# Optimization experiments

Measured on AMD Instinct MI355X. Metric: run time of the kernel, lower is better.

The kernel has to match this reference:

```python
import jax, jax.numpy as jnp
import numpy as np

EMB = 256
HEADS = 8

def setup_inputs() -> dict:
    key = jax.random.key(0)
    ks = jax.random.split(key, 8)
    b, t, e, h = 8, 1024, EMB, HEADS
    x = jax.random.normal(ks[0], (b, t, e), dtype=jnp.float32)
    mask_idx = jax.random.randint(ks[1], (b, t, 1), 0, 2, dtype=jnp.int32)
    s = 1.0 / np.sqrt(e)
    Wq = jax.random.normal(ks[2], (e, e * h), dtype=jnp.float32) * s
    Wk = jax.random.normal(ks[3], (e, e * h), dtype=jnp.float32) * s
    Wv = jax.random.normal(ks[4], (e, e * h), dtype=jnp.float32) * s
    Wu = jax.random.normal(ks[5], (h * e, e), dtype=jnp.float32) * (1.0 / np.sqrt(h * e))
    bu = jnp.zeros((e,), dtype=jnp.float32)
    return {"x": x, "mask_idx": mask_idx, "Wq": Wq, "Wk": Wk, "Wv": Wv, "Wu": Wu, "bu": bu}

def reference(x, mask_idx, Wq, Wk, Wv, Wu, bu):
    b, t, e = x.shape
    h = HEADS
    # project and split heads: (b,t,h,e) -> (b,h,t,e)
    q = (x @ Wq).reshape(b, t, h, e).transpose(0, 2, 1, 3)
    k = (x @ Wk).reshape(b, t, h, e).transpose(0, 2, 1, 3)
    v = (x @ Wv).reshape(b, t, h, e).transpose(0, 2, 1, 3)
    scale = e ** 0.25
    q = q / scale
    k = k / scale
    dot = jnp.einsum('bhte,bhse->bhts', q, k)  # (b,h,t,t)
    m = mask_idx.astype(x.dtype)  # (b,t,1)
    mm = jnp.einsum('bti,bsi->bts', m, m)[:, None]  # (b,1,t,t), outer-product mask
    attn = jax.nn.softmax(dot * mm + (1.0 - mm) * (-1e30), axis=-1)
    out = jnp.einsum('bhts,bhse->bhte', attn, v)  # (b,h,t,e)
    out = out.transpose(0, 2, 1, 3).reshape(b, t, h * e)
    return out @ Wu + bu
```

## Files before the change

### kernel.cpp

```cpp
#include <hip/hip_runtime.h>

#define BB 8
#define TT 1024
#define EE 256
#define HH 8
#define BH 64
#define MM 8192
#define NQKV 2048

typedef __attribute__((ext_vector_type(8))) short bf16x8;
typedef __attribute__((ext_vector_type(4))) float f32x4;

__device__ __forceinline__ unsigned short f2bf(float f) {
  unsigned int u = __float_as_uint(f);
  u += 0x7fff + ((u >> 16) & 1);
  return (unsigned short)(u >> 16);
}

__global__ void k_convert_x(const float4* __restrict__ x, ushort4* __restrict__ xb, int n4) {
  int i = blockIdx.x * 256 + threadIdx.x;
  if (i < n4) {
    float4 f = x[i];
    ushort4 o;
    o.x = f2bf(f.x); o.y = f2bf(f.y); o.z = f2bf(f.z); o.w = f2bf(f.w);
    xb[i] = o;
  }
}

__global__ void k_transpose_w(const float* __restrict__ in, unsigned short* __restrict__ out,
                              int K, int N, float scale) {
  __shared__ float tile[32][33];
  int n0 = blockIdx.x * 32, k0 = blockIdx.y * 32;
  int tx = threadIdx.x & 31, ty = threadIdx.x >> 5;
#pragma unroll
  for (int p = 0; p < 4; p++) tile[ty + 8 * p][tx] = in[(size_t)(k0 + ty + 8 * p) * N + (n0 + tx)];
  __syncthreads();
#pragma unroll
  for (int p = 0; p < 4; p++)
    out[(size_t)(n0 + ty + 8 * p) * K + (k0 + tx)] = f2bf(scale * tile[tx][ty + 8 * p]);
}

__global__ __launch_bounds__(256) void k_gemm_qkv(
    const unsigned short* __restrict__ xb,
    const unsigned short* __restrict__ Wtq,
    const unsigned short* __restrict__ Wtk,
    const unsigned short* __restrict__ Wtv,
    unsigned short* __restrict__ qo,
    unsigned short* __restrict__ ko,
    unsigned short* __restrict__ vto) {
  __shared__ unsigned short sh[2 * 128 * 72];
  unsigned short* As = sh;
  unsigned short* Bs = sh + 128 * 72;
  const unsigned short* Bw = (blockIdx.z == 0) ? Wtq : (blockIdx.z == 1 ? Wtk : Wtv);
  int tid = threadIdx.x, lane = tid & 63, w = tid >> 6;
  int wr = w >> 1, wc = w & 1;
  int m0 = blockIdx.y * 128, n0 = blockIdx.x * 128;
  f32x4 acc[4][4] = {};
  for (int kt = 0; kt < 4; kt++) {
    __syncthreads();
    const unsigned short* ga = xb + (size_t)m0 * 256 + kt * 64;
    const unsigned short* gb = Bw + (size_t)n0 * 256 + kt * 64;
#pragma unroll
    for (int p = 0; p < 4; p++) {
      int c = p * 256 + tid, row = c >> 3, col = (c & 7) * 8;
      *(bf16x8*)&As[row * 72 + col] = *(const bf16x8*)&ga[(size_t)row * 256 + col];
      *(bf16x8*)&Bs[row * 72 + col] = *(const bf16x8*)&gb[(size_t)row * 256 + col];
    }
    __syncthreads();
#pragma unroll
    for (int kk = 0; kk < 2; kk++) {
      bf16x8 af[4], bfr[4];
#pragma unroll
      for (int mi = 0; mi < 4; mi++)
        af[mi] = *(bf16x8*)&As[(wr * 64 + mi * 16 + (lane & 15)) * 72 + kk * 32 + (lane >> 4) * 8];
#pragma unroll
      for (int ni = 0; ni < 4; ni++)
        bfr[ni] = *(bf16x8*)&Bs[(wc * 64 + ni * 16 + (lane & 15)) * 72 + kk * 32 + (lane >> 4) * 8];
#pragma unroll
      for (int mi = 0; mi < 4; mi++)
#pragma unroll
        for (int ni = 0; ni < 4; ni++)
          acc[mi][ni] = __builtin_amdgcn_mfma_f32_16x16x32_bf16(af[mi], bfr[ni], acc[mi][ni], 0, 0, 0);
    }
  }
  __syncthreads();
  unsigned short* ob = sh + w * (64 * 72);
  int gm0 = m0 + wr * 64, gn0 = n0 + wc * 64;
  int bb = gm0 >> 10, t0 = gm0 & 1023, hh = gn0 >> 8, d0 = gn0 & 255;
  if (blockIdx.z != 2) {
#pragma unroll
    for (int mi = 0; mi < 4; mi++)
#pragma unroll
      for (int ni = 0; ni < 4; ni++)
#pragma unroll
        for (int i = 0; i < 4; i++)
          ob[(mi * 16 + (lane >> 4) * 4 + i) * 72 + ni * 16 + (lane & 15)] = f2bf(acc[mi][ni][i]);
    unsigned short* outp = (blockIdx.z == 0) ? qo : ko;
    unsigned short* dst = outp + ((size_t)(bb * HH + hh) * TT + t0) * EE + d0;
#pragma unroll
    for (int p = 0; p < 8; p++) {
      int row = (lane >> 3) + 8 * p, col = (lane & 7) * 8;
      *(bf16x8*)&dst[(size_t)row * EE + col] = *(bf16x8*)&ob[row * 72 + col];
    }
  } else {
#pragma unroll
    for (int mi = 0; mi < 4; mi++)
#pragma unroll
      for (int ni = 0; ni < 4; ni++)
#pragma unroll
        for (int i = 0; i < 4; i++)
          ob[(ni * 16 + (lane & 15)) * 72 + mi * 16 + (lane >> 4) * 4 + i] = f2bf(acc[mi][ni][i]);
    unsigned short* dst = vto + ((size_t)(bb * HH + hh) * EE + d0) * TT + t0;
#pragma unroll
    for (int p = 0; p < 8; p++) {
      int row = (lane >> 3) + 8 * p, col = (lane & 7) * 8;
      *(bf16x8*)&dst[(size_t)row * TT + col] = *(bf16x8*)&ob[row * 72 + col];
    }
  }
}

__global__ __launch_bounds__(256, 2) void k_flash(
    const unsigned short* __restrict__ q,
    const unsigned short* __restrict__ k,
    const unsigned short* __restrict__ vt,
    const int* __restrict__ mask,
    unsigned short* __restrict__ ao) {
  __shared__ unsigned short Ks[64 * 264];
  __shared__ unsigned short Vs[256 * 72];
  __shared__ unsigned short Ps[4 * 16 * 72];
  int tid = threadIdx.x, lane = tid & 63, w = tid >> 6;
  int L = blockIdx.x;
  int wg = (L & 7) * 128 + (L >> 3);
  int qt = wg & 15, bh = wg >> 4;
  int b = bh >> 3, hh = bh & 7;
  const unsigned short* qbase = q + ((size_t)bh * TT + qt * 64) * EE;
  const unsigned short* kbase = k + (size_t)bh * TT * EE;
  const unsigned short* vbase = vt + (size_t)bh * EE * TT;

#pragma unroll
  for (int p = 0; p < 8; p++) {
    int c = p * 256 + tid, row = c >> 5, col = (c & 31) * 8;
    *(bf16x8*)&Ks[row * 264 + col] = *(const bf16x8*)&qbase[(size_t)row * EE + col];
  }
  __syncthreads();
  bf16x8 qr[8];
#pragma unroll
  for (int kk = 0; kk < 8; kk++)
    qr[kk] = *(bf16x8*)&Ks[(w * 16 + (lane & 15)) * 264 + kk * 32 + (lane >> 4) * 8];

  int mq[4];
#pragma unroll
  for (int i = 0; i < 4; i++)
    mq[i] = mask[b * TT + qt * 64 + w * 16 + (lane >> 4) * 4 + i];

  float mrow[4], lrow[4];
  f32x4 oacc[16] = {};
#pragma unroll
  for (int i = 0; i < 4; i++) { mrow[i] = -1e30f; lrow[i] = 0.0f; }

  for (int kt = 0; kt < 16; kt++) {
    __syncthreads();
#pragma unroll
    for (int p = 0; p < 8; p++) {
      int c = p * 256 + tid, row = c >> 5, col = (c & 31) * 8;
      *(bf16x8*)&Ks[row * 264 + col] = *(const bf16x8*)&kbase[((size_t)(kt * 64 + row)) * EE + col];
    }
#pragma unroll
    for (int p = 0; p < 8; p++) {
      int c = p * 256 + tid, d = c >> 3, col = (c & 7) * 8;
      *(bf16x8*)&Vs[d * 72 + col] = *(const bf16x8*)&vbase[(size_t)d * TT + kt * 64 + col];
    }
    __syncthreads();

    f32x4 sacc[4] = {};
#pragma unroll
    for (int kk = 0; kk < 8; kk++) {
#pragma unroll
      for (int fc = 0; fc < 4; fc++) {
        bf16x8 bfr = *(bf16x8*)&Ks[(fc * 16 + (lane & 15)) * 264 + kk * 32 + (lane >> 4) * 8];
        sacc[fc] = __builtin_amdgcn_mfma_f32_16x16x32_bf16(qr[kk], bfr, sacc[fc], 0, 0, 0);
      }
    }

    int msv[4];
#pragma unroll
    for (int fc = 0; fc < 4; fc++) msv[fc] = mask[b * TT + kt * 64 + fc * 16 + (lane & 15)];
    float pv[4][4], rmax[4];
#pragma unroll
    for (int i = 0; i < 4; i++) rmax[i] = -1e30f;
#pragma unroll
    for (int fc = 0; fc < 4; fc++)
#pragma unroll
      for (int i = 0; i < 4; i++) {
        float s = (mq[i] && msv[fc]) ? sacc[fc][i] : -1e30f;
        pv[fc][i] = s;
        rmax[i] = fmaxf(rmax[i], s);
      }
#pragma unroll
    for (int off = 1; off < 16; off <<= 1)
#pragma unroll
      for (int i = 0; i < 4; i++) rmax[i] = fmaxf(rmax[i], __shfl_xor(rmax[i], off));
    bool need = false;
#pragma unroll
    for (int i = 0; i < 4; i++) need |= (rmax[i] - mrow[i] > 8.0f);
    if (__any(need)) {
      float sc[4];
#pragma unroll
      for (int i = 0; i < 4; i++) {
        float mn = fmaxf(mrow[i], rmax[i]);
        sc[i] = __expf(mrow[i] - mn);
        mrow[i] = mn;
        lrow[i] *= sc[i];
      }
#pragma unroll
      for (int f = 0; f < 16; f++)
#pragma unroll
        for (int i = 0; i < 4; i++) oacc[f][i] *= sc[i];
    }
    float rsum[4] = {0.f, 0.f, 0.f, 0.f};
#pragma unroll
    for (int fc = 0; fc < 4; fc++)
#pragma unroll
      for (int i = 0; i < 4; i++) {
        float pe = __expf(pv[fc][i] - mrow[i]);
        pv[fc][i] = pe;
        rsum[i] += pe;
      }
#pragma unroll
    for (int off = 1; off < 16; off <<= 1)
#pragma unroll
      for (int i = 0; i < 4; i++) rsum[i] += __shfl_xor(rsum[i], off);
#pragma unroll
    for (int i = 0; i < 4; i++) lrow[i] += rsum[i];

    unsigned short* Pw = Ps + w * (16 * 72);
#pragma unroll
    for (int fc = 0; fc < 4; fc++)
#pragma unroll
      for (int i = 0; i < 4; i++)
        Pw[((lane >> 4) * 4 + i) * 72 + fc * 16 + (lane & 15)] = f2bf(pv[fc][i]);
#pragma unroll
    for (int kk2 = 0; kk2 < 2; kk2++) {
      bf16x8 pa = *(bf16x8*)&Pw[(lane & 15) * 72 + kk2 * 32 + (lane >> 4) * 8];
#pragma unroll
      for (int ff = 0; ff < 16; ff++) {
        bf16x8 vb = *(bf16x8*)&Vs[(ff * 16 + (lane & 15)) * 72 + kk2 * 32 + (lane >> 4) * 8];
        oacc[ff] = __builtin_amdgcn_mfma_f32_16x16x32_bf16(pa, vb, oacc[ff], 0, 0, 0);
      }
    }
  }

  float inv[4];
#pragma unroll
  for (int i = 0; i < 4; i++) inv[i] = 1.0f / lrow[i];
#pragma unroll
  for (int f = 0; f < 16; f++)
#pragma unroll
    for (int i = 0; i < 4; i++) oacc[f][i] *= inv[i];
  unsigned short* Pw = Ps + w * (16 * 72);
  int t0 = qt * 64 + w * 16;
#pragma unroll
  for (int c = 0; c < 4; c++) {
#pragma unroll
    for (int f4 = 0; f4 < 4; f4++) {
      int f = c * 4 + f4;
#pragma unroll
      for (int i = 0; i < 4; i++)
        Pw[((lane >> 4) * 4 + i) * 72 + f4 * 16 + (lane & 15)] = f2bf(oacc[f][i]);
    }
#pragma unroll
    for (int p = 0; p < 2; p++) {
      int row = lane >> 2, col = ((lane & 3) * 2 + p) * 8;
      bf16x8 vv = *(bf16x8*)&Pw[row * 72 + col];
      *(bf16x8*)&ao[((size_t)(b * TT + t0 + row)) * NQKV + hh * EE + c * 64 + col] = vv;
    }
  }
}

__global__ __launch_bounds__(256) void k_gemm_out(
    const unsigned short* __restrict__ A,
    const unsigned short* __restrict__ Wut,
    const float* __restrict__ bu,
    float* __restrict__ out) {
  __shared__ unsigned short As[128 * 72];
  __shared__ unsigned short Bs[64 * 72];
  int tid = threadIdx.x, lane = tid & 63, w = tid >> 6;
  int wr = w >> 1, wc = w & 1;
  int m0 = blockIdx.y * 128, n0 = blockIdx.x * 64;
  f32x4 acc[4][2] = {};
  for (int kt = 0; kt < 32; kt++) {
    __syncthreads();
    const unsigned short* ga = A + (size_t)m0 * 2048 + kt * 64;
    const unsigned short* gb = Wut + (size_t)n0 * 2048 + kt * 64;
#pragma unroll
    for (int p = 0; p < 4; p++) {
      int c = p * 256 + tid, row = c >> 3, col = (c & 7) * 8;
      *(bf16x8*)&As[row * 72 + col] = *(const bf16x8*)&ga[(size_t)row * 2048 + col];
    }
#pragma unroll
    for (int p = 0; p < 2; p++) {
      int c = p * 256 + tid, row = c >> 3, col = (c & 7) * 8;
      *(bf16x8*)&Bs[row * 72 + col] = *(const bf16x8*)&gb[(size_t)row * 2048 + col];
    }
    __syncthreads();
#pragma unroll
    for (int kk = 0; kk < 2; kk++) {
      bf16x8 af[4], bfr[2];
#pragma unroll
      for (int mi = 0; mi < 4; mi++)
        af[mi] = *(bf16x8*)&As[(wr * 64 + mi * 16 + (lane & 15)) * 72 + kk * 32 + (lane >> 4) * 8];
#pragma unroll
      for (int ni = 0; ni < 2; ni++)
        bfr[ni] = *(bf16x8*)&Bs[(wc * 32 + ni * 16 + (lane & 15)) * 72 + kk * 32 + (lane >> 4) * 8];
#pragma unroll
      for (int mi = 0; mi < 4; mi++)
#pragma unroll
        for (int ni = 0; ni < 2; ni++)
          acc[mi][ni] = __builtin_amdgcn_mfma_f32_16x16x32_bf16(af[mi], bfr[ni], acc[mi][ni], 0, 0, 0);
    }
  }
#pragma unroll
  for (int mi = 0; mi < 4; mi++)
#pragma unroll
    for (int ni = 0; ni < 2; ni++) {
      int gm = m0 + wr * 64 + mi * 16 + (lane >> 4) * 4;
      int gn = n0 + wc * 32 + ni * 16 + (lane & 15);
      float bias = bu[gn];
#pragma unroll
      for (int i = 0; i < 4; i++)
        out[(size_t)(gm + i) * EE + gn] = acc[mi][ni][i] + bias;
    }
}

extern "C" void kernel_launch(void* const* d_in, const int* in_sizes, int n_in,
                              void* d_out, int out_size, void* d_ws, size_t ws_size,
                              hipStream_t stream) {
  const float* x  = (const float*)d_in[0];
  const int* mask = (const int*)d_in[1];
  const float* Wq = (const float*)d_in[2];
  const float* Wk = (const float*)d_in[3];
  const float* Wv = (const float*)d_in[4];
  const float* Wu = (const float*)d_in[5];
  const float* bu = (const float*)d_in[6];
  float* out = (float*)d_out;

  char* ws = (char*)d_ws;
  size_t off = 0;
  auto alloc = [&](size_t bytes) {
    char* p = ws + off;
    off += (bytes + 255) & ~(size_t)255;
    return p;
  };
  unsigned short* xb  = (unsigned short*)alloc((size_t)MM * EE * 2);
  unsigned short* Wtq = (unsigned short*)alloc((size_t)NQKV * EE * 2);
  unsigned short* Wtk = (unsigned short*)alloc((size_t)NQKV * EE * 2);
  unsigned short* Wtv = (unsigned short*)alloc((size_t)NQKV * EE * 2);
  unsigned short* Wut = (unsigned short*)alloc((size_t)EE * NQKV * 2);
  unsigned short* qb  = (unsigned short*)alloc((size_t)BH * TT * EE * 2);
  unsigned short* kb  = (unsigned short*)alloc((size_t)BH * TT * EE * 2);
  unsigned short* vtb = (unsigned short*)alloc((size_t)BH * TT * EE * 2);
  unsigned short* ao  = (unsigned short*)alloc((size_t)MM * NQKV * 2);

  hipLaunchKernelGGL(k_convert_x, dim3((MM * EE / 4 + 255) / 256), dim3(256), 0, stream,
                     (const float4*)x, (ushort4*)xb, MM * EE / 4);
  hipLaunchKernelGGL(k_transpose_w, dim3(NQKV / 32, EE / 32), dim3(256), 0, stream, Wq, Wtq, EE, NQKV, 0.25f);
  hipLaunchKernelGGL(k_transpose_w, dim3(NQKV / 32, EE / 32), dim3(256), 0, stream, Wk, Wtk, EE, NQKV, 0.25f);
  hipLaunchKernelGGL(k_transpose_w, dim3(NQKV / 32, EE / 32), dim3(256), 0, stream, Wv, Wtv, EE, NQKV, 1.0f);
  hipLaunchKernelGGL(k_transpose_w, dim3(EE / 32, NQKV / 32), dim3(256), 0, stream, Wu, Wut, NQKV, EE, 1.0f);

  hipLaunchKernelGGL(k_gemm_qkv, dim3(NQKV / 128, MM / 128, 3), dim3(256), 0, stream,
                     xb, Wtq, Wtk, Wtv, qb, kb, vtb);
  hipLaunchKernelGGL(k_flash, dim3(TT / 64 * BH), dim3(256), 0, stream, qb, kb, vtb, mask, ao);
  hipLaunchKernelGGL(k_gemm_out, dim3(EE / 64, MM / 128), dim3(256), 0, stream, ao, Wut, bu, out);
}
```

Baseline: 335.6 us.

## Double-buffer K/V tiles in flash kernel with register prefetch; merge weight transposes

Shrinks the flash-attention KV tile from 64 to 32 keys and double-buffers K and V in shared memory. The next tile is prefetched into registers while the current one is computed, so only one barrier per iteration remains. The four weight-transpose launches are also merged into a single kernel to cut launch overhead. Smaller tiles double the number of loop iterations and the softmax reduction overhead, and the prefetch registers raise register pressure at 2 blocks per SM.

```diff
diff --git a/kernel.cpp b/kernel.cpp
--- a/kernel.cpp
+++ b/kernel.cpp
@@ -27,10 +27,20 @@
   }
 }
 
-__global__ void k_transpose_w(const float* __restrict__ in, unsigned short* __restrict__ out,
-                              int K, int N, float scale) {
+__global__ void k_prep_w(const float* __restrict__ Wq, const float* __restrict__ Wk,
+                         const float* __restrict__ Wv, const float* __restrict__ Wu,
+                         unsigned short* __restrict__ Wtq, unsigned short* __restrict__ Wtk,
+                         unsigned short* __restrict__ Wtv, unsigned short* __restrict__ Wut) {
   __shared__ float tile[32][33];
-  int n0 = blockIdx.x * 32, k0 = blockIdx.y * 32;
+  int z = blockIdx.y;
+  const float* in = (z == 0) ? Wq : (z == 1) ? Wk : (z == 2) ? Wv : Wu;
+  unsigned short* out = (z == 0) ? Wtq : (z == 1) ? Wtk : (z == 2) ? Wtv : Wut;
+  int K = (z < 3) ? EE : NQKV;
+  int N = (z < 3) ? NQKV : EE;
+  float scale = (z < 2) ? 0.25f : 1.0f;
+  int nb = N / 32;
+  int bx = blockIdx.x % nb, by = blockIdx.x / nb;
+  int n0 = bx * 32, k0 = by * 32;
   int tx = threadIdx.x & 31, ty = threadIdx.x >> 5;
 #pragma unroll
   for (int p = 0; p < 4; p++) tile[ty + 8 * p][tx] = in[(size_t)(k0 + ty + 8 * p) * N + (n0 + tx)];
@@ -119,15 +129,17 @@
   }
 }
 
+#define KV 32
+#define NT (TT / KV)
 __global__ __launch_bounds__(256, 2) void k_flash(
     const unsigned short* __restrict__ q,
     const unsigned short* __restrict__ k,
     const unsigned short* __restrict__ vt,
     const int* __restrict__ mask,
     unsigned short* __restrict__ ao) {
-  __shared__ unsigned short Ks[64 * 264];
-  __shared__ unsigned short Vs[256 * 72];
-  __shared__ unsigned short Ps[4 * 16 * 72];
+  __shared__ unsigned short Ks[2 * 32 * 264];
+  __shared__ unsigned short Vs[2 * 256 * 40];
+  __shared__ unsigned short Ps[4 * 16 * 40];
   int tid = threadIdx.x, lane = tid & 63, w = tid >> 6;
   int L = blockIdx.x;
   int wg = (L & 7) * 128 + (L >> 3);
@@ -137,6 +149,13 @@
   const unsigned short* kbase = k + (size_t)bh * TT * EE;
   const unsigned short* vbase = vt + (size_t)bh * EE * TT;
 
+  bf16x8 kpre[4], vpre[4];
+#pragma unroll
+  for (int p = 0; p < 4; p++) {
+    int c = p * 256 + tid;
+    kpre[p] = *(const bf16x8*)&kbase[(size_t)(c >> 5) * EE + (c & 31) * 8];
+    vpre[p] = *(const bf16x8*)&vbase[(size_t)(c >> 2) * TT + (c & 3) * 8];
+  }
 #pragma unroll
   for (int p = 0; p < 8; p++) {
     int c = p * 256 + tid, row = c >> 5, col = (c & 31) * 8;
@@ -147,6 +166,14 @@
 #pragma unroll
   for (int kk = 0; kk < 8; kk++)
     qr[kk] = *(bf16x8*)&Ks[(w * 16 + (lane & 15)) * 264 + kk * 32 + (lane >> 4) * 8];
+  __syncthreads();
+#pragma unroll
+  for (int p = 0; p < 4; p++) {
+    int c = p * 256 + tid;
+    *(bf16x8*)&Ks[(c >> 5) * 264 + (c & 31) * 8] = kpre[p];
+    *(bf16x8*)&Vs[(c >> 2) * 40 + (c & 3) * 8] = vpre[p];
+  }
+  __syncthreads();
 
   int mq[4];
 #pragma unroll
@@ -158,38 +185,37 @@
 #pragma unroll
   for (int i = 0; i < 4; i++) { mrow[i] = -1e30f; lrow[i] = 0.0f; }
 
-  for (int kt = 0; kt < 16; kt++) {
-    __syncthreads();
-#pragma unroll
-    for (int p = 0; p < 8; p++) {
-      int c = p * 256 + tid, row = c >> 5, col = (c & 31) * 8;
-      *(bf16x8*)&Ks[row * 264 + col] = *(const bf16x8*)&kbase[((size_t)(kt * 64 + row)) * EE + col];
-    }
-#pragma unroll
-    for (int p = 0; p < 8; p++) {
-      int c = p * 256 + tid, d = c >> 3, col = (c & 7) * 8;
-      *(bf16x8*)&Vs[d * 72 + col] = *(const bf16x8*)&vbase[(size_t)d * TT + kt * 64 + col];
-    }
-    __syncthreads();
-
-    f32x4 sacc[4] = {};
+  int cur = 0;
+  for (int kt = 0; kt < NT; kt++) {
+    if (kt < NT - 1) {
+#pragma unroll
+      for (int p = 0; p < 4; p++) {
+        int c = p * 256 + tid;
+        kpre[p] = *(const bf16x8*)&kbase[(size_t)((kt + 1) * KV + (c >> 5)) * EE + (c & 31) * 8];
+        vpre[p] = *(const bf16x8*)&vbase[(size_t)(c >> 2) * TT + (kt + 1) * KV + (c & 3) * 8];
+      }
+    }
+    const unsigned short* Kc = Ks + cur * (32 * 264);
+    const unsigned short* Vc = Vs + cur * (256 * 40);
+
+    f32x4 sacc[2] = {};
 #pragma unroll
     for (int kk = 0; kk < 8; kk++) {
 #pragma unroll
-      for (int fc = 0; fc < 4; fc++) {
-        bf16x8 bfr = *(bf16x8*)&Ks[(fc * 16 + (lane & 15)) * 264 + kk * 32 + (lane >> 4) * 8];
+      for (int fc = 0; fc < 2; fc++) {
+        bf16x8 bfr = *(const bf16x8*)&Kc[(fc * 16 + (lane & 15)) * 264 + kk * 32 + (lane >> 4) * 8];
         sacc[fc] = __builtin_amdgcn_mfma_f32_16x16x32_bf16(qr[kk], bfr, sacc[fc], 0, 0, 0);
       }
     }
 
-    int msv[4];
-#pragma unroll
-    for (int fc = 0; fc < 4; fc++) msv[fc] = mask[b * TT + kt * 64 + fc * 16 + (lane & 15)];
-    float pv[4][4], rmax[4];
+    int msv[2];
+#pragma unroll
+    for (int fc = 0; fc < 2; fc++) msv[fc] = mask[b * TT + kt * KV + fc * 16 + (lane & 15)];
+    float pv[2][4], rmax[4];
 #pragma unroll
     for (int i = 0; i < 4; i++) rmax[i] = -1e30f;
 #pragma unroll
-    for (int fc = 0; fc < 4; fc++)
+    for (int fc = 0; fc < 2; fc++)
 #pragma unroll
       for (int i = 0; i < 4; i++) {
         float s = (mq[i] && msv[fc]) ? sacc[fc][i] : -1e30f;
@@ -219,7 +245,7 @@
     }
     float rsum[4] = {0.f, 0.f, 0.f, 0.f};
 #pragma unroll
-    for (int fc = 0; fc < 4; fc++)
+    for (int fc = 0; fc < 2; fc++)
 #pragma unroll
       for (int i = 0; i < 4; i++) {
         float pe = __expf(pv[fc][i] - mrow[i]);
@@ -233,21 +259,31 @@
 #pragma unroll
     for (int i = 0; i < 4; i++) lrow[i] += rsum[i];
 
-    unsigned short* Pw = Ps + w * (16 * 72);
-#pragma unroll
-    for (int fc = 0; fc < 4; fc++)
+    unsigned short* Pw = Ps + w * (16 * 40);
+#pragma unroll
+    for (int fc = 0; fc < 2; fc++)
 #pragma unroll
       for (int i = 0; i < 4; i++)
-        Pw[((lane >> 4) * 4 + i) * 72 + fc * 16 + (lane & 15)] = f2bf(pv[fc][i]);
-#pragma unroll
-    for (int kk2 = 0; kk2 < 2; kk2++) {
-      bf16x8 pa = *(bf16x8*)&Pw[(lane & 15) * 72 + kk2 * 32 + (lane >> 4) * 8];
-#pragma unroll
-      for (int ff = 0; ff < 16; ff++) {
-        bf16x8 vb = *(bf16x8*)&Vs[(ff * 16 + (lane & 15)) * 72 + kk2 * 32 + (lane >> 4) * 8];
-        oacc[ff] = __builtin_amdgcn_mfma_f32_16x16x32_bf16(pa, vb, oacc[ff], 0, 0, 0);
-      }
-    }
+        Pw[((lane >> 4) * 4 + i) * 40 + fc * 16 + (lane & 15)] = f2bf(pv[fc][i]);
+    bf16x8 pa = *(const bf16x8*)&Pw[(lane & 15) * 40 + (lane >> 4) * 8];
+#pragma unroll
+    for (int ff = 0; ff < 16; ff++) {
+      bf16x8 vb = *(const bf16x8*)&Vc[(ff * 16 + (lane & 15)) * 40 + (lane >> 4) * 8];
+      oacc[ff] = __builtin_amdgcn_mfma_f32_16x16x32_bf16(pa, vb, oacc[ff], 0, 0, 0);
+    }
+
+    if (kt < NT - 1) {
+      unsigned short* Kn = Ks + (cur ^ 1) * (32 * 264);
+      unsigned short* Vn = Vs + (cur ^ 1) * (256 * 40);
+#pragma unroll
+      for (int p = 0; p < 4; p++) {
+        int c = p * 256 + tid;
+        *(bf16x8*)&Kn[(c >> 5) * 264 + (c & 31) * 8] = kpre[p];
+        *(bf16x8*)&Vn[(c >> 2) * 40 + (c & 3) * 8] = vpre[p];
+      }
+      __syncthreads();
+    }
+    cur ^= 1;
   }
 
   float inv[4];
@@ -257,23 +293,20 @@
   for (int f = 0; f < 16; f++)
 #pragma unroll
     for (int i = 0; i < 4; i++) oacc[f][i] *= inv[i];
-  unsigned short* Pw = Ps + w * (16 * 72);
+  unsigned short* Pw = Ps + w * (16 * 40);
   int t0 = qt * 64 + w * 16;
 #pragma unroll
-  for (int c = 0; c < 4; c++) {
-#pragma unroll
-    for (int f4 = 0; f4 < 4; f4++) {
-      int f = c * 4 + f4;
+  for (int c2 = 0; c2 < 8; c2++) {
+#pragma unroll
+    for (int f2 = 0; f2 < 2; f2++) {
+      int f = c2 * 2 + f2;
 #pragma unroll
       for (int i = 0; i < 4; i++)
-        Pw[((lane >> 4) * 4 + i) * 72 + f4 * 16 + (lane & 15)] = f2bf(oacc[f][i]);
-    }
-#pragma unroll
-    for (int p = 0; p < 2; p++) {
-      int row = lane >> 2, col = ((lane & 3) * 2 + p) * 8;
-      bf16x8 vv = *(bf16x8*)&Pw[row * 72 + col];
-      *(bf16x8*)&ao[((size_t)(b * TT + t0 + row)) * NQKV + hh * EE + c * 64 + col] = vv;
-    }
+        Pw[((lane >> 4) * 4 + i) * 40 + f2 * 16 + (lane & 15)] = f2bf(oacc[f][i]);
+    }
+    int row = lane >> 2, colg = (lane & 3) * 8;
+    bf16x8 vv = *(const bf16x8*)&Pw[row * 40 + colg];
+    *(bf16x8*)&ao[((size_t)(b * TT + t0 + row)) * NQKV + hh * EE + c2 * 32 + colg] = vv;
   }
 }
 
@@ -363,10 +396,8 @@
 
   hipLaunchKernelGGL(k_convert_x, dim3((MM * EE / 4 + 255) / 256), dim3(256), 0, stream,
                      (const float4*)x, (ushort4*)xb, MM * EE / 4);
-  hipLaunchKernelGGL(k_transpose_w, dim3(NQKV / 32, EE / 32), dim3(256), 0, stream, Wq, Wtq, EE, NQKV, 0.25f);
-  hipLaunchKernelGGL(k_transpose_w, dim3(NQKV / 32, EE / 32), dim3(256), 0, stream, Wk, Wtk, EE, NQKV, 0.25f);
-  hipLaunchKernelGGL(k_transpose_w, dim3(NQKV / 32, EE / 32), dim3(256), 0, stream, Wv, Wtv, EE, NQKV, 1.0f);
-  hipLaunchKernelGGL(k_transpose_w, dim3(EE / 32, NQKV / 32), dim3(256), 0, stream, Wu, Wut, NQKV, EE, 1.0f);
+  hipLaunchKernelGGL(k_prep_w, dim3(512, 4), dim3(256), 0, stream,
+                     Wq, Wk, Wv, Wu, Wtq, Wtk, Wtv, Wut);
 
   hipLaunchKernelGGL(k_gemm_qkv, dim3(NQKV / 128, MM / 128, 3), dim3(256), 0, stream,
                      xb, Wtq, Wtk, Wtv, qb, kb, vtb);
```

After: 343.8 us. 1.02x slower.
